# Optimization experiments

Hardware: AMD Instinct MI355X
Metric: run time of the kernel (lower is better)

Reference implementation:

```python
import jax, jax.numpy as jnp
import numpy as np
from jax import lax

B, C, H, W = 2, 256, 64, 64
CI = C // 2           # inter_channels = 128
CH = CI // 2          # key/query channels = 64
EPS = 1e-5


def conv1x1(x, w, b):
    # x: [B,C,H,W], w: [O,C], b: [O]
    return jnp.einsum('oc,bchw->bohw', w, x) + b[None, :, None, None]


def bn(x, g, be, m, v):
    inv = (g / jnp.sqrt(v + EPS))[None, :, None, None]
    return (x - m[None, :, None, None]) * inv + be[None, :, None, None]


def setup_inputs() -> dict:
    key = jax.random.key(0)
    ks = jax.random.split(key, 40)
    r = lambda i, shape, sc=0.05: jax.random.normal(ks[i], shape, dtype=jnp.float32) * sc
    u = lambda i, shape: jax.random.uniform(ks[i], shape, dtype=jnp.float32, minval=0.5, maxval=1.5)
    return {
        'q': jax.random.normal(ks[0], (B, C, H, W), dtype=jnp.float32),
        's': jax.random.normal(ks[1], (B, C, H, W), dtype=jnp.float32),
        'scale': jnp.full((1,), 0.3, dtype=jnp.float32),
        'w_v': r(2, (CI, C)), 'b_v': r(3, (CI,)),
        'w_k1': r(4, (CH, C)), 'b_k1': r(5, (CH,)),
        'w_q1': r(6, (CH, C)), 'b_q1': r(7, (CH,)),
        'w_k2': r(8, (CH, C)), 'b_k2': r(9, (CH,)),
        'w_q2': r(10, (CH, C)), 'b_q2': r(11, (CH,)),
        'w_ts': r(12, (CI, C)), 'b_ts': r(13, (CI,)),
        'g_ts': u(14, (CI,)), 'be_ts': r(15, (CI,)), 'm_ts': r(16, (CI,)), 'v_ts': u(17, (CI,)),
        'w_tq': r(18, (CI, C)), 'b_tq': r(19, (CI,)),
        'g_tq': u(20, (CI,)), 'be_tq': r(21, (CI,)), 'm_tq': r(22, (CI,)), 'v_tq': u(23, (CI,)),
        'w_cat': r(24, (CI, 2 * CI, 3, 3)),
        'g_cat': u(25, (CI,)), 'be_cat': r(26, (CI,)), 'm_cat': r(27, (CI,)), 'v_cat': u(28, (CI,)),
    }


def reference(q, s, scale, w_v, b_v, w_k1, b_k1, w_q1, b_q1, w_k2, b_k2, w_q2, b_q2,
              w_ts, b_ts, g_ts, be_ts, m_ts, v_ts,
              w_tq, b_tq, g_tq, be_tq, m_tq, v_tq,
              w_cat, g_cat, be_cat, m_cat, v_cat):
    b_, _, h, w = q.shape
    n = h * w
    # values: [B, N, CI]
    v_q = conv1x1(q, w_v, b_v).reshape(b_, CI, n).transpose(0, 2, 1)
    v_s = conv1x1(s, w_v, b_v).reshape(b_, CI, n).transpose(0, 2, 1)
    # concatenated keys/queries: [B, CI, N]
    k_x = jnp.concatenate([conv1x1(q, w_k1, b_k1), conv1x1(s, w_k2, b_k2)], axis=1).reshape(b_, CI, n)
    q_x = jnp.concatenate([conv1x1(q, w_q1, b_q1), conv1x1(s, w_q2, b_q2)], axis=1).reshape(b_, CI, n)
    # affinity: [B, N, N]
    A_s = jnp.einsum('bcn,bcm->bnm', k_x, q_x)
    attn_s = jax.nn.softmax(A_s, axis=-1)
    attn_q = jax.nn.softmax(jnp.transpose(A_s, (0, 2, 1)), axis=-1)
    # p_s: [B, N, CI] -> [B, CI, H, W]
    p_s = jnp.einsum('bnm,bmc->bnc', attn_s, v_s).transpose(0, 2, 1).reshape(b_, CI, h, w)
    s_t = bn(conv1x1(s, w_ts, b_ts), g_ts, be_ts, m_ts, v_ts)
    q_t = bn(conv1x1(q, w_tq, b_tq), g_tq, be_tq, m_tq, v_tq)
    E_s = scale[0] * p_s + s_t
    q_s_ = jnp.einsum('bnm,bmc->bnc', attn_q, v_q).transpose(0, 2, 1).reshape(b_, CI, h, w)
    E_q = scale[0] * q_s_ + q_t
    cat = jnp.concatenate([E_q, E_s], axis=1)
    conv = lax.conv_general_dilated(cat, w_cat, (1, 1), 'SAME',
                                    dimension_numbers=('NCHW', 'OIHW', 'NCHW'))
    cpam = jax.nn.relu(bn(conv, g_cat, be_cat, m_cat, v_cat))
    return (cpam, E_q, E_s)
```

## Files before the change

kernel.cpp:

```cpp
#include <hip/hip_runtime.h>
#include <hip/hip_bf16.h>

#define NPIX 4096
#define NCH  256
#define CI   128
#define EPS  1e-5f
#define SOFF 20.0f

typedef unsigned short u16;
typedef __attribute__((ext_vector_type(8))) short short8;
typedef __attribute__((ext_vector_type(4))) float f32x4;

__device__ __forceinline__ float bfu2f(u16 u) {
    union { unsigned int i; float f; } x; x.i = ((unsigned int)u) << 16; return x.f;
}
__device__ __forceinline__ u16 f2bfu(float f) {
    union { float ff; unsigned int i; } x; x.ff = f;
    unsigned int r = x.i + 0x7FFFu + ((x.i >> 16) & 1u);
    return (u16)(r >> 16);
}

__device__ __forceinline__ void gload16(const u16* g, u16* l) {
    __builtin_amdgcn_global_load_lds(
        (const __attribute__((address_space(1))) unsigned int*)g,
        (__attribute__((address_space(3))) unsigned int*)l,
        16, 0, 0);
}

__global__ __launch_bounds__(256) void prep_kernel(
    const float* __restrict__ w_v,
    const float* __restrict__ w_k1, const float* __restrict__ w_q1,
    const float* __restrict__ w_k2, const float* __restrict__ w_q2,
    const float* __restrict__ w_ts, const float* __restrict__ w_tq,
    u16* __restrict__ Wbf,
    const float* __restrict__ w_cat, u16* __restrict__ wT)
{
    const int bx = blockIdx.x;
    if (bx < 768) {
        int idx = bx * 256 + threadIdx.x;
        int src = idx / 98304;
        int r   = idx - src * 98304;
        int o   = r >> 8, c = r & 255;
        float v;
        if (o < 128)      v = w_v[(size_t)o * 256 + c];
        else if (o < 192) v = (src ? w_k2 : w_k1)[(size_t)(o - 128) * 256 + c];
        else if (o < 256) v = (src ? w_q2 : w_q1)[(size_t)(o - 192) * 256 + c];
        else              v = (src ? w_ts : w_tq)[(size_t)(o - 256) * 256 + c];
        Wbf[idx] = f2bfu(v);
    } else {
        int co = bx - 768;
        const float* srcb = w_cat + (size_t)co * 2304;
        u16* dstb = wT + (size_t)co * 2304;
        for (int t = threadIdx.x; t < 2304; t += 256) {
            int ic = t / 9, tap = t - ic * 9;
            dstb[tap * 256 + ic] = f2bfu(srcb[t]);
        }
    }
}

__global__ __launch_bounds__(256) void proj2_kernel(
    const float* __restrict__ xq, const float* __restrict__ xs,
    const u16* __restrict__ Wbf,
    const float* __restrict__ b_v,
    const float* __restrict__ b_k1, const float* __restrict__ b_q1,
    const float* __restrict__ b_k2, const float* __restrict__ b_q2,
    const float* __restrict__ b_ts, const float* __restrict__ g_ts,
    const float* __restrict__ be_ts, const float* __restrict__ m_ts,
    const float* __restrict__ v_ts,
    const float* __restrict__ b_tq, const float* __restrict__ g_tq,
    const float* __restrict__ be_tq, const float* __restrict__ m_tq,
    const float* __restrict__ v_tq,
    u16* __restrict__ kT, u16* __restrict__ qT,
    u16* __restrict__ vq, u16* __restrict__ vs,
    u16* __restrict__ tq, u16* __restrict__ ts)
{
    __shared__ u16 Xs[64 * 264];
    __shared__ u16 KQ[64 * 136];

    const int tid  = threadIdx.x;
    const int lane = tid & 63;
    const int wid  = tid >> 6;
    const int l16  = lane & 15;
    const int quad = lane >> 4;

    const int n0  = blockIdx.x * 64;
    const int bz  = blockIdx.z;
    const int b   = bz >> 1, src = bz & 1;

    const float* xg = (src ? xs : xq) + (size_t)b * NCH * NPIX + n0;
    #pragma unroll
    for (int k0 = 0; k0 < 64; k0 += 16) {
        float v[16];
        #pragma unroll
        for (int k = 0; k < 16; ++k) {
            int idx = tid + (k0 + k) * 256;
            int c = idx >> 6, n = idx & 63;
            v[k] = xg[(size_t)c * NPIX + n];
        }
        #pragma unroll
        for (int k = 0; k < 16; ++k) {
            int idx = tid + (k0 + k) * 256;
            int c = idx >> 6, n = idx & 63;
            Xs[n * 264 + c] = f2bfu(v[k]);
        }
    }
    __syncthreads();

    const u16* W = Wbf + (size_t)src * 384 * 256;
    const int o0w = wid * 96;
    const float* bk = src ? b_k2 : b_k1;
    const float* bq = src ? b_q2 : b_q1;
    const float* bt = src ? b_ts : b_tq;

    f32x4 acc[24];
    #pragma unroll
    for (int ot = 0; ot < 6; ++ot) {
        int ob = o0w + ot * 16 + quad * 4;
        const float* bp;
        if (ob < 128)      bp = b_v + ob;
        else if (ob < 192) bp = bk + (ob - 128);
        else if (ob < 256) bp = bq + (ob - 192);
        else               bp = bt + (ob - 256);
        float4 b4 = *(const float4*)bp;
        f32x4 iv = (f32x4){b4.x, b4.y, b4.z, b4.w};
        #pragma unroll
        for (int pt = 0; pt < 4; ++pt) acc[ot * 4 + pt] = iv;
    }

    #pragma unroll
    for (int kc = 0; kc < 8; ++kc) {
        short8 bfr[4];
        #pragma unroll
        for (int pt = 0; pt < 4; ++pt)
            bfr[pt] = *(const short8*)&Xs[(pt * 16 + l16) * 264 + kc * 32 + quad * 8];
        #pragma unroll
        for (int ot = 0; ot < 6; ++ot) {
            short8 a = *(const short8*)&W[(size_t)(o0w + ot * 16 + l16) * 256 + kc * 32 + quad * 8];
            #pragma unroll
            for (int pt = 0; pt < 4; ++pt)
                acc[ot * 4 + pt] = __builtin_amdgcn_mfma_f32_16x16x32_bf16(a, bfr[pt], acc[ot * 4 + pt], 0, 0, 0);
        }
    }

    #pragma unroll
    for (int ot = 0; ot < 6; ++ot) {
        int ob = o0w + ot * 16;
        #pragma unroll
        for (int pt = 0; pt < 4; ++pt) {
            int px = pt * 16 + l16;
            f32x4 v4 = acc[ot * 4 + pt];
            if (ob < 128) {
                u16* dst = src ? vs : vq;
                #pragma unroll
                for (int r = 0; r < 4; ++r)
                    dst[((size_t)b * CI + ob + quad * 4 + r) * NPIX + n0 + px] = f2bfu(v4[r]);
            } else if (ob < 256) {
                int colb = (ob < 192) ? (ob - 128) : (64 + ob - 192);
                #pragma unroll
                for (int r = 0; r < 4; ++r)
                    KQ[px * 136 + colb + quad * 4 + r] = f2bfu(v4[r]);
            } else {
                const float* g  = src ? g_ts  : g_tq;
                const float* be = src ? be_ts : be_tq;
                const float* mm = src ? m_ts  : m_tq;
                const float* vv = src ? v_ts  : v_tq;
                u16* dst = src ? ts : tq;
                #pragma unroll
                for (int r = 0; r < 4; ++r) {
                    int oc = ob - 256 + quad * 4 + r;
                    float inv = g[oc] * rsqrtf(vv[oc] + EPS);
                    dst[((size_t)b * CI + oc) * NPIX + n0 + px] =
                        f2bfu((v4[r] - mm[oc]) * inv + be[oc]);
                }
            }
        }
    }
    __syncthreads();

    const int chb = src ? 64 : 0;
    #pragma unroll
    for (int u = 0; u < 4; ++u) {
        int idx = tid + u * 256;
        int px = idx >> 4, oct = idx & 15;
        uint4 val = *(const uint4*)&KQ[px * 136 + oct * 8];
        if (oct < 8)
            *(uint4*)&kT[((size_t)b * NPIX + n0 + px) * CI + chb + oct * 8] = val;
        else
            *(uint4*)&qT[((size_t)b * NPIX + n0 + px) * CI + chb + (oct - 8) * 8] = val;
    }
}

#define AKS_OFF 0
#define AVT_OFF 16384
#define APS_OFF 32768
#define ASMEM_U16 37376

__global__ __launch_bounds__(256) void attn_kernel(
    const u16* __restrict__ kT, const u16* __restrict__ qT,
    const u16* __restrict__ vq, const u16* __restrict__ vs,
    u16* __restrict__ Opart, float* __restrict__ Lpart, int nseg)
{
    __shared__ __align__(16) u16 smem[ASMEM_U16];
    u16* Ps = smem + APS_OFF;

    const int tid  = threadIdx.x;
    const int lane = tid & 63;
    const int wid  = tid >> 6;
    const int l16  = lane & 15;
    const int quad = lane >> 4;
    const int strip = wid * 16;

    const int nt = blockIdx.x;
    const int n0 = nt * 64;
    const int at = blockIdx.y;
    const int z  = blockIdx.z;
    const int b  = z / nseg;
    const int seg = z - b * nseg;

    const u16* Qg = at ? qT : kT;
    const u16* Kg = at ? kT : qT;
    const u16* Vg = at ? vq : vs;

    short8 qf[4];
    {
        const u16* Qb = Qg + ((size_t)b * NPIX + n0 + strip + l16) * CI;
        #pragma unroll
        for (int kc = 0; kc < 4; ++kc)
            qf[kc] = *(const short8*)&Qb[kc * 32 + quad * 8];
    }

    f32x4 o[8];
    #pragma unroll
    for (int ct = 0; ct < 8; ++ct) o[ct] = (f32x4){0.f, 0.f, 0.f, 0.f};
    float L = 0.f;

    const u16* KgB = Kg + (size_t)b * NPIX * CI;
    const u16* VgB = Vg + (size_t)b * CI * NPIX;

    const int mt0 = seg * (64 / nseg);
    const int mt1 = mt0 + (64 / nseg);

    #define ISSUE_TILE(buf, m0_)                                              \
    {                                                                         \
        u16* kb_ = smem + AKS_OFF + (buf) * 8192;                             \
        u16* vb_ = smem + AVT_OFF + (buf) * 8192;                             \
        _Pragma("unroll")                                                     \
        for (int k = 0; k < 4; ++k) {                                         \
            int sb  = k * 256 + wid * 64;                                     \
            int idx = sb + lane;                                              \
            int row = idx >> 4, segp = idx & 15;                              \
            int segg = segp ^ (row & 15);                                     \
            gload16(KgB + (size_t)((m0_) + row) * CI + segg * 8, kb_ + sb * 8); \
        }                                                                     \
        _Pragma("unroll")                                                     \
        for (int k = 0; k < 4; ++k) {                                         \
            int sb  = k * 256 + wid * 64;                                     \
            int idx = sb + lane;                                              \
            int c = idx >> 3, sgp = idx & 7;                                  \
            int sgg = sgp ^ (c & 7);                                          \
            gload16(VgB + (size_t)c * NPIX + (m0_) + sgg * 8, vb_ + sb * 8);  \
        }                                                                     \
    }

    int cur = 0;
    ISSUE_TILE(0, mt0 * 64);

    for (int mt = mt0; mt < mt1; ++mt) {
        __syncthreads();
        if (mt + 1 < mt1) ISSUE_TILE(1 - cur, (mt + 1) * 64);

        const u16* Ks = smem + AKS_OFF + cur * 8192;
        const u16* Vt = smem + AVT_OFF + cur * 8192;

        f32x4 sv[4];
        #pragma unroll
        for (int m2 = 0; m2 < 4; ++m2) {
            f32x4 c = (f32x4){0.f, 0.f, 0.f, 0.f};
            #pragma unroll
            for (int kc = 0; kc < 4; ++kc) {
                int s = kc * 4 + quad;
                short8 kf = *(const short8*)&Ks[(m2 * 16 + l16) * 128 + ((s ^ l16) * 8)];
                c = __builtin_amdgcn_mfma_f32_16x16x32_bf16(kf, qf[kc], c, 0, 0, 0);
            }
            sv[m2] = c;
        }

        float Lsum = 0.f;
        u16* myPs = Ps + (strip + l16) * 72;
        #pragma unroll
        for (int m2 = 0; m2 < 4; ++m2) {
            float p0 = __expf(sv[m2][0] - SOFF);
            float p1 = __expf(sv[m2][1] - SOFF);
            float p2 = __expf(sv[m2][2] - SOFF);
            float p3 = __expf(sv[m2][3] - SOFF);
            Lsum += (p0 + p1) + (p2 + p3);
            ushort4 pk;
            pk.x = f2bfu(p0); pk.y = f2bfu(p1);
            pk.z = f2bfu(p2); pk.w = f2bfu(p3);
            *(ushort4*)&myPs[m2 * 16 + quad * 4] = pk;
        }
        Lsum += __shfl_xor(Lsum, 16);
        Lsum += __shfl_xor(Lsum, 32);
        L += Lsum;

        short8 ap[2];
        #pragma unroll
        for (int kc = 0; kc < 2; ++kc)
            ap[kc] = *(const short8*)&Ps[(strip + l16) * 72 + kc * 32 + quad * 8];
        #pragma unroll
        for (int ct = 0; ct < 8; ++ct) {
            #pragma unroll
            for (int kc = 0; kc < 2; ++kc) {
                int s = kc * 4 + quad;
                short8 bv = *(const short8*)&Vt[(ct * 16 + l16) * 64 + ((s ^ (l16 & 7)) * 8)];
                o[ct] = __builtin_amdgcn_mfma_f32_16x16x32_bf16(ap[kc], bv, o[ct], 0, 0, 0);
            }
        }
        cur ^= 1;
    }

    const size_t tile = (((size_t)(at * 2 + b) * 64 + nt) * nseg + seg);
    u16* Ob = Opart + tile * 8192;
    #pragma unroll
    for (int r = 0; r < 4; ++r) {
        int row = strip + quad * 4 + r;
        #pragma unroll
        for (int ct = 0; ct < 8; ++ct)
            Ob[row * 128 + ct * 16 + l16] = f2bfu(o[ct][r]);
    }
    if (quad == 0)
        Lpart[tile * 64 + strip + l16] = L;
    #undef ISSUE_TILE
}

__global__ __launch_bounds__(256) void attn_combine_kernel(
    const u16* __restrict__ Opart, const float* __restrict__ Lpart,
    const u16* __restrict__ tq, const u16* __restrict__ ts,
    const float* __restrict__ scale_p,
    float* __restrict__ out, u16* __restrict__ Ebf, int nseg)
{
    __shared__ float Of[128 * 68];
    __shared__ float invL[64];

    const int tid = threadIdx.x;
    const int nt = blockIdx.x;
    const int n0 = nt * 64;
    const int at = blockIdx.y;
    const int b  = blockIdx.z;

    const u16* Tg = at ? tq : ts;
    float* outE   = out + (size_t)(at ? 1 : 2) * 1048576;
    const int ch0 = at ? 0 : 128;
    const size_t tbase = ((size_t)(at * 2 + b) * 64 + nt) * nseg;

    if (tid < 64) {
        float Lg = 0.f;
        for (int s = 0; s < nseg; ++s) Lg += Lpart[(tbase + s) * 64 + tid];
        invL[tid] = 1.f / Lg;
    }
    __syncthreads();

    #pragma unroll
    for (int k = 0; k < 4; ++k) {
        int idx = tid + k * 256;
        int row = idx >> 4, oct = idx & 15;
        float m[8] = {0.f, 0.f, 0.f, 0.f, 0.f, 0.f, 0.f, 0.f};
        for (int s = 0; s < nseg; ++s) {
            union { uint4 v; u16 u[8]; } pk;
            pk.v = *(const uint4*)&Opart[(tbase + s) * 8192 + row * 128 + oct * 8];
            #pragma unroll
            for (int j = 0; j < 8; ++j) m[j] += bfu2f(pk.u[j]);
        }
        float w = invL[row];
        #pragma unroll
        for (int j = 0; j < 8; ++j)
            Of[(oct * 8 + j) * 68 + row] = m[j] * w;
    }
    __syncthreads();

    float scale = *scale_p;
    const u16* Tb = Tg + (size_t)b * CI * NPIX + n0;
    float* Ob = outE + (size_t)b * CI * NPIX + n0;
    for (int idx = tid; idx < 128 * 64; idx += 256) {
        int c = idx >> 6, r = idx & 63;
        float v = scale * Of[c * 68 + r] + bfu2f(Tb[(size_t)c * NPIX + r]);
        Ob[(size_t)c * NPIX + r] = v;
        Ebf[((size_t)b * NPIX + n0 + r) * NCH + ch0 + c] = f2bfu(v);
    }
}

#define CXT_STR 40

__global__ __launch_bounds__(256) void conv_kernel(
    const u16* __restrict__ Ebf,
    const u16* __restrict__ wT,
    const float* __restrict__ g_cat, const float* __restrict__ be_cat,
    const float* __restrict__ m_cat, const float* __restrict__ v_cat,
    float* __restrict__ out)
{
    __shared__ u16 XtW[4][3 * 34 * CXT_STR];

    const int tid  = threadIdx.x;
    const int lane = tid & 63;
    const int wid  = tid >> 6;
    const int l16  = lane & 15;
    const int quad = lane >> 4;

    const int h    = blockIdx.x;
    const int coff = blockIdx.y * 32;
    const int b    = blockIdx.z;

    const int cot = wid >> 1;
    const int pxt = (wid & 1) * 2;
    const int gc0 = pxt * 16 - 1;

    f32x4 acc[2];
    #pragma unroll
    for (int j = 0; j < 2; ++j) acc[j] = (f32x4){0.f, 0.f, 0.f, 0.f};

    const u16* Eb = Ebf + (size_t)b * NPIX * NCH;
    u16* Xw = &XtW[wid][0];
    const int cobase = coff + cot * 16 + l16;

    for (int icc = 0; icc < 8; ++icc) {
        const int ic0 = icc * 32;

        short8 wfrag[9];
        #pragma unroll
        for (int tap = 0; tap < 9; ++tap)
            wfrag[tap] = *(const short8*)&wT[((size_t)cobase * 9 + tap) * 256 + ic0 + quad * 8];

        for (int u = lane; u < 408; u += 64) {
            int part = u & 3, xe = u >> 2;
            int dh = xe / 34, x = xe - dh * 34;
            int gr = h + dh - 1, gc = gc0 + x;
            uint4 val = make_uint4(0u, 0u, 0u, 0u);
            if ((unsigned)gr < 64u && (unsigned)gc < 64u)
                val = *(const uint4*)&Eb[((size_t)gr * 64 + gc) * NCH + ic0 + part * 8];
            *(uint4*)&Xw[(dh * 34 + x) * CXT_STR + part * 8] = val;
        }

        #pragma unroll
        for (int tap = 0; tap < 9; ++tap) {
            const int dh = tap / 3, dw = tap % 3;
            short8 bf[2];
            #pragma unroll
            for (int j = 0; j < 2; ++j) {
                int x = j * 16 + l16 + dw;
                bf[j] = *(const short8*)&Xw[(dh * 34 + x) * CXT_STR + quad * 8];
            }
            #pragma unroll
            for (int j = 0; j < 2; ++j)
                acc[j] = __builtin_amdgcn_mfma_f32_16x16x32_bf16(wfrag[tap], bf[j], acc[j], 0, 0, 0);
        }
    }

    #pragma unroll
    for (int r = 0; r < 4; ++r) {
        int co = coff + cot * 16 + quad * 4 + r;
        float inv = g_cat[co] * rsqrtf(v_cat[co] + EPS);
        float mm  = m_cat[co];
        float be  = be_cat[co];
        #pragma unroll
        for (int j = 0; j < 2; ++j) {
            int wcol = (pxt + j) * 16 + l16;
            float v = (acc[j][r] - mm) * inv + be;
            out[((size_t)b * CI + co) * NPIX + h * 64 + wcol] = fmaxf(v, 0.f);
        }
    }
}

extern "C" void kernel_launch(void* const* d_in, const int* in_sizes, int n_in,
                              void* d_out, int out_size, void* d_ws, size_t ws_size,
                              hipStream_t stream)
{
    const float* q     = (const float*)d_in[0];
    const float* s     = (const float*)d_in[1];
    const float* scale = (const float*)d_in[2];
    const float* w_v   = (const float*)d_in[3];
    const float* b_v   = (const float*)d_in[4];
    const float* w_k1  = (const float*)d_in[5];
    const float* b_k1  = (const float*)d_in[6];
    const float* w_q1  = (const float*)d_in[7];
    const float* b_q1  = (const float*)d_in[8];
    const float* w_k2  = (const float*)d_in[9];
    const float* b_k2  = (const float*)d_in[10];
    const float* w_q2  = (const float*)d_in[11];
    const float* b_q2  = (const float*)d_in[12];
    const float* w_ts  = (const float*)d_in[13];
    const float* b_ts  = (const float*)d_in[14];
    const float* g_ts  = (const float*)d_in[15];
    const float* be_ts = (const float*)d_in[16];
    const float* m_ts  = (const float*)d_in[17];
    const float* v_ts  = (const float*)d_in[18];
    const float* w_tq  = (const float*)d_in[19];
    const float* b_tq  = (const float*)d_in[20];
    const float* g_tq  = (const float*)d_in[21];
    const float* be_tq = (const float*)d_in[22];
    const float* m_tq  = (const float*)d_in[23];
    const float* v_tq  = (const float*)d_in[24];
    const float* w_cat = (const float*)d_in[25];
    const float* g_cat = (const float*)d_in[26];
    const float* be_cat= (const float*)d_in[27];
    const float* m_cat = (const float*)d_in[28];
    const float* v_cat = (const float*)d_in[29];

    float* out = (float*)d_out;
    u16* ws = (u16*)d_ws;
    const size_t SZ = (size_t)2 * CI * NPIX;
    u16* kT  = ws;
    u16* qT  = kT + SZ;
    u16* vq  = qT + SZ;
    u16* vs  = vq + SZ;
    u16* tq  = vs + SZ;
    u16* ts  = tq + SZ;
    u16* Wbf = ts + SZ;
    u16* B   = Wbf + 196608;
    u16* Ebf = B;
    u16* wTc = B + 2097152;
    u16* Opart = wTc + 294912;

    const size_t fixed_u16 = 6 * SZ + 196608 + 2097152 + 294912;
    int nseg = 1;
    {
        size_t need4 = (fixed_u16 + (size_t)4 * 2097152) * 2 + (size_t)4 * 131072;
        size_t need2 = (fixed_u16 + (size_t)2 * 2097152) * 2 + (size_t)2 * 131072;
        if (ws_size >= need4)      nseg = 4;
        else if (ws_size >= need2) nseg = 2;
    }
    float* Lpart = (float*)(Opart + (size_t)nseg * 256 * 8192);

    dim3 blk(256);
    hipLaunchKernelGGL(prep_kernel, dim3(896), blk, 0, stream,
                       w_v, w_k1, w_q1, w_k2, w_q2, w_ts, w_tq, Wbf, w_cat, wTc);
    hipLaunchKernelGGL(proj2_kernel, dim3(64, 1, 4), blk, 0, stream,
                       q, s, Wbf, b_v, b_k1, b_q1, b_k2, b_q2,
                       b_ts, g_ts, be_ts, m_ts, v_ts,
                       b_tq, g_tq, be_tq, m_tq, v_tq,
                       kT, qT, vq, vs, tq, ts);
    hipLaunchKernelGGL(attn_kernel, dim3(64, 2, 2 * nseg), blk, 0, stream,
                       kT, qT, vq, vs, Opart, Lpart, nseg);
    hipLaunchKernelGGL(attn_combine_kernel, dim3(64, 2, 2), blk, 0, stream,
                       Opart, Lpart, tq, ts, scale, out, Ebf, nseg);
    hipLaunchKernelGGL(conv_kernel, dim3(64, 4, 2), blk, 0, stream,
                       Ebf, wTc, g_cat, be_cat, m_cat, v_cat, out);
}
```

Before: 243.0 us.

## Switch attention to 32x32x16 MFMA with 2x2 wave tiling and coalesce E store

The attention kernel moves from 16x16x32 to 32x32x16 bf16 MFMA. Each wave now computes a 32-row by 32-key score block and a 32-row by 64-channel output block, rather than a 16-row strip over all keys and channels. The goal is fewer MFMA issues and fewer LDS fragment loads per FLOP. The cost is an extra __syncthreads per tile so waves can share the P matrix, plus an LDS reduction of the row sums across wave pairs. The combine kernel also stages E in shared memory so the bf16 pixel-major output is written with coalesced channel-contiguous stores.

```diff
diff --git a/kernel.cpp b/kernel.cpp
--- a/kernel.cpp
+++ b/kernel.cpp
@@ -10,6 +10,7 @@
 typedef unsigned short u16;
 typedef __attribute__((ext_vector_type(8))) short short8;
 typedef __attribute__((ext_vector_type(4))) float f32x4;
+typedef __attribute__((ext_vector_type(16))) float f32x16;
 
 __device__ __forceinline__ float bfu2f(u16 u) {
     union { unsigned int i; float f; } x; x.i = ((unsigned int)u) << 16; return x.f;
@@ -195,20 +196,24 @@
 #define APS_OFF 32768
 #define ASMEM_U16 37376
 
-__global__ __launch_bounds__(256) void attn_kernel(
+__global__ __launch_bounds__(256, 2) void attn_kernel(
     const u16* __restrict__ kT, const u16* __restrict__ qT,
     const u16* __restrict__ vq, const u16* __restrict__ vs,
     u16* __restrict__ Opart, float* __restrict__ Lpart, int nseg)
 {
     __shared__ __align__(16) u16 smem[ASMEM_U16];
+    __shared__ float Lbuf[2][2][32];
     u16* Ps = smem + APS_OFF;
 
     const int tid  = threadIdx.x;
     const int lane = tid & 63;
     const int wid  = tid >> 6;
-    const int l16  = lane & 15;
-    const int quad = lane >> 4;
-    const int strip = wid * 16;
+    const int l32  = lane & 31;
+    const int hi   = lane >> 5;
+    const int rg   = wid >> 1;
+    const int mh   = wid & 1;
+    const int chb  = (wid & 1) * 64;
+    const int rows0 = rg * 32;
 
     const int nt = blockIdx.x;
     const int n0 = nt * 64;
@@ -221,18 +226,20 @@
     const u16* Kg = at ? kT : qT;
     const u16* Vg = at ? vq : vs;
 
-    short8 qf[4];
+    short8 qf[8];
     {
-        const u16* Qb = Qg + ((size_t)b * NPIX + n0 + strip + l16) * CI;
-        #pragma unroll
-        for (int kc = 0; kc < 4; ++kc)
-            qf[kc] = *(const short8*)&Qb[kc * 32 + quad * 8];
-    }
-
-    f32x4 o[8];
-    #pragma unroll
-    for (int ct = 0; ct < 8; ++ct) o[ct] = (f32x4){0.f, 0.f, 0.f, 0.f};
-    float L = 0.f;
+        const u16* Qb = Qg + ((size_t)b * NPIX + n0 + rows0 + l32) * CI;
+        #pragma unroll
+        for (int kc = 0; kc < 8; ++kc)
+            qf[kc] = *(const short8*)&Qb[kc * 16 + hi * 8];
+    }
+
+    f32x16 o2[2];
+    #pragma unroll
+    for (int ct = 0; ct < 2; ++ct)
+        #pragma unroll
+        for (int i = 0; i < 16; ++i) o2[ct][i] = 0.f;
+    float Lacc = 0.f;
 
     const u16* KgB = Kg + (size_t)b * NPIX * CI;
     const u16* VgB = Vg + (size_t)b * CI * NPIX;
@@ -272,48 +279,49 @@
         const u16* Ks = smem + AKS_OFF + cur * 8192;
         const u16* Vt = smem + AVT_OFF + cur * 8192;
 
-        f32x4 sv[4];
-        #pragma unroll
-        for (int m2 = 0; m2 < 4; ++m2) {
-            f32x4 c = (f32x4){0.f, 0.f, 0.f, 0.f};
-            #pragma unroll
-            for (int kc = 0; kc < 4; ++kc) {
-                int s = kc * 4 + quad;
-                short8 kf = *(const short8*)&Ks[(m2 * 16 + l16) * 128 + ((s ^ l16) * 8)];
-                c = __builtin_amdgcn_mfma_f32_16x16x32_bf16(kf, qf[kc], c, 0, 0, 0);
+        f32x16 sv;
+        #pragma unroll
+        for (int i = 0; i < 16; ++i) sv[i] = 0.f;
+        {
+            const int row = mh * 32 + l32;
+            #pragma unroll
+            for (int kc = 0; kc < 8; ++kc) {
+                int sg = (kc * 2 + hi) ^ (row & 15);
+                short8 kf = *(const short8*)&Ks[row * 128 + sg * 8];
+                sv = __builtin_amdgcn_mfma_f32_32x32x16_bf16(kf, qf[kc], sv, 0, 0, 0);
             }
-            sv[m2] = c;
-        }
-
-        float Lsum = 0.f;
-        u16* myPs = Ps + (strip + l16) * 72;
-        #pragma unroll
-        for (int m2 = 0; m2 < 4; ++m2) {
-            float p0 = __expf(sv[m2][0] - SOFF);
-            float p1 = __expf(sv[m2][1] - SOFF);
-            float p2 = __expf(sv[m2][2] - SOFF);
-            float p3 = __expf(sv[m2][3] - SOFF);
-            Lsum += (p0 + p1) + (p2 + p3);
+        }
+
+        float Ls = 0.f;
+        u16* myPs = Ps + (rows0 + l32) * 72 + mh * 32;
+        #pragma unroll
+        for (int rq = 0; rq < 4; ++rq) {
+            float p0 = __expf(sv[rq * 4 + 0] - SOFF);
+            float p1 = __expf(sv[rq * 4 + 1] - SOFF);
+            float p2 = __expf(sv[rq * 4 + 2] - SOFF);
+            float p3 = __expf(sv[rq * 4 + 3] - SOFF);
+            Ls += (p0 + p1) + (p2 + p3);
             ushort4 pk;
             pk.x = f2bfu(p0); pk.y = f2bfu(p1);
             pk.z = f2bfu(p2); pk.w = f2bfu(p3);
-            *(ushort4*)&myPs[m2 * 16 + quad * 4] = pk;
-        }
-        Lsum += __shfl_xor(Lsum, 16);
-        Lsum += __shfl_xor(Lsum, 32);
-        L += Lsum;
-
-        short8 ap[2];
-        #pragma unroll
-        for (int kc = 0; kc < 2; ++kc)
-            ap[kc] = *(const short8*)&Ps[(strip + l16) * 72 + kc * 32 + quad * 8];
-        #pragma unroll
-        for (int ct = 0; ct < 8; ++ct) {
-            #pragma unroll
-            for (int kc = 0; kc < 2; ++kc) {
-                int s = kc * 4 + quad;
-                short8 bv = *(const short8*)&Vt[(ct * 16 + l16) * 64 + ((s ^ (l16 & 7)) * 8)];
-                o[ct] = __builtin_amdgcn_mfma_f32_16x16x32_bf16(ap[kc], bv, o[ct], 0, 0, 0);
+            *(ushort4*)&myPs[rq * 8 + hi * 4] = pk;
+        }
+        Ls += __shfl_xor(Ls, 32);
+        Lacc += Ls;
+        __syncthreads();
+
+        short8 pf[4];
+        #pragma unroll
+        for (int kc = 0; kc < 4; ++kc)
+            pf[kc] = *(const short8*)&Ps[(rows0 + l32) * 72 + kc * 16 + hi * 8];
+        #pragma unroll
+        for (int ct = 0; ct < 2; ++ct) {
+            const int c = chb + ct * 32 + l32;
+            #pragma unroll
+            for (int kc = 0; kc < 4; ++kc) {
+                int slot = (kc * 2 + hi) ^ (c & 7);
+                short8 vf = *(const short8*)&Vt[c * 64 + slot * 8];
+                o2[ct] = __builtin_amdgcn_mfma_f32_32x32x16_bf16(vf, pf[kc], o2[ct], 0, 0, 0);
             }
         }
         cur ^= 1;
@@ -321,15 +329,25 @@
 
     const size_t tile = (((size_t)(at * 2 + b) * 64 + nt) * nseg + seg);
     u16* Ob = Opart + tile * 8192;
-    #pragma unroll
-    for (int r = 0; r < 4; ++r) {
-        int row = strip + quad * 4 + r;
-        #pragma unroll
-        for (int ct = 0; ct < 8; ++ct)
-            Ob[row * 128 + ct * 16 + l16] = f2bfu(o[ct][r]);
-    }
-    if (quad == 0)
-        Lpart[tile * 64 + strip + l16] = L;
+    {
+        const int row = rows0 + l32;
+        #pragma unroll
+        for (int ct = 0; ct < 2; ++ct) {
+            #pragma unroll
+            for (int rq = 0; rq < 4; ++rq) {
+                ushort4 pk;
+                pk.x = f2bfu(o2[ct][rq * 4 + 0]);
+                pk.y = f2bfu(o2[ct][rq * 4 + 1]);
+                pk.z = f2bfu(o2[ct][rq * 4 + 2]);
+                pk.w = f2bfu(o2[ct][rq * 4 + 3]);
+                *(ushort4*)&Ob[row * 128 + chb + ct * 32 + rq * 8 + hi * 4] = pk;
+            }
+        }
+    }
+    if (hi == 0) Lbuf[rg][mh][l32] = Lacc;
+    __syncthreads();
+    if (mh == 0 && hi == 0)
+        Lpart[tile * 64 + rows0 + l32] = Lbuf[rg][0][l32] + Lbuf[rg][1][l32];
     #undef ISSUE_TILE
 }
 
@@ -385,7 +403,13 @@
         int c = idx >> 6, r = idx & 63;
         float v = scale * Of[c * 68 + r] + bfu2f(Tb[(size_t)c * NPIX + r]);
         Ob[(size_t)c * NPIX + r] = v;
-        Ebf[((size_t)b * NPIX + n0 + r) * NCH + ch0 + c] = f2bfu(v);
+        Of[c * 68 + r] = v;
+    }
+    __syncthreads();
+    u16* Eb = Ebf + ((size_t)b * NPIX + n0) * NCH + ch0;
+    for (int idx = tid; idx < 128 * 64; idx += 256) {
+        int r = idx >> 7, c = idx & 127;
+        Eb[(size_t)r * NCH + c] = f2bfu(Of[c * 68 + r]);
     }
 }
 
```

Measured after the change: 248.5 us. 2.3% more time.

## Split projection, combine and conv kernels into more, smaller blocks

Applied to the files above, without the earlier changes.

Splits the projection kernel's output channels across two blocks, one producing keys and the other queries, and halves the row tile in the combine kernel. The combine kernel also now stages its results in shared memory so the bf16 channel-last writes to Ebf are coalesced. The conv kernel gives each block 16 output channels and each wave one 16-pixel strip. The aim is more blocks per kernel to fill the GPU's compute units, plus better-coalesced stores. In exchange, each input tile is reloaded by more blocks and per-wave reuse of conv weights and inputs drops.

```diff
diff --git a/kernel.cpp b/kernel.cpp
--- a/kernel.cpp
+++ b/kernel.cpp
@@ -75,7 +75,7 @@
     u16* __restrict__ tq, u16* __restrict__ ts)
 {
     __shared__ u16 Xs[64 * 264];
-    __shared__ u16 KQ[64 * 136];
+    __shared__ u16 KQ[64 * 72];
 
     const int tid  = threadIdx.x;
     const int lane = tid & 63;
@@ -84,6 +84,7 @@
     const int quad = lane >> 4;
 
     const int n0  = blockIdx.x * 64;
+    const int oh  = blockIdx.y;
     const int bz  = blockIdx.z;
     const int b   = bz >> 1, src = bz & 1;
 
@@ -107,14 +108,14 @@
     __syncthreads();
 
     const u16* W = Wbf + (size_t)src * 384 * 256;
-    const int o0w = wid * 96;
+    const int o0w = oh * 192 + wid * 48;
     const float* bk = src ? b_k2 : b_k1;
     const float* bq = src ? b_q2 : b_q1;
     const float* bt = src ? b_ts : b_tq;
 
-    f32x4 acc[24];
-    #pragma unroll
-    for (int ot = 0; ot < 6; ++ot) {
+    f32x4 acc[12];
+    #pragma unroll
+    for (int ot = 0; ot < 3; ++ot) {
         int ob = o0w + ot * 16 + quad * 4;
         const float* bp;
         if (ob < 128)      bp = b_v + ob;
@@ -134,7 +135,7 @@
         for (int pt = 0; pt < 4; ++pt)
             bfr[pt] = *(const short8*)&Xs[(pt * 16 + l16) * 264 + kc * 32 + quad * 8];
         #pragma unroll
-        for (int ot = 0; ot < 6; ++ot) {
+        for (int ot = 0; ot < 3; ++ot) {
             short8 a = *(const short8*)&W[(size_t)(o0w + ot * 16 + l16) * 256 + kc * 32 + quad * 8];
             #pragma unroll
             for (int pt = 0; pt < 4; ++pt)
@@ -143,7 +144,7 @@
     }
 
     #pragma unroll
-    for (int ot = 0; ot < 6; ++ot) {
+    for (int ot = 0; ot < 3; ++ot) {
         int ob = o0w + ot * 16;
         #pragma unroll
         for (int pt = 0; pt < 4; ++pt) {
@@ -155,10 +156,10 @@
                 for (int r = 0; r < 4; ++r)
                     dst[((size_t)b * CI + ob + quad * 4 + r) * NPIX + n0 + px] = f2bfu(v4[r]);
             } else if (ob < 256) {
-                int colb = (ob < 192) ? (ob - 128) : (64 + ob - 192);
+                int colb = (ob < 192) ? (ob - 128) : (ob - 192);
                 #pragma unroll
                 for (int r = 0; r < 4; ++r)
-                    KQ[px * 136 + colb + quad * 4 + r] = f2bfu(v4[r]);
+                    KQ[px * 72 + colb + quad * 4 + r] = f2bfu(v4[r]);
             } else {
                 const float* g  = src ? g_ts  : g_tq;
                 const float* be = src ? be_ts : be_tq;
@@ -177,16 +178,14 @@
     }
     __syncthreads();
 
+    u16* KQdst = oh ? qT : kT;
     const int chb = src ? 64 : 0;
     #pragma unroll
-    for (int u = 0; u < 4; ++u) {
+    for (int u = 0; u < 2; ++u) {
         int idx = tid + u * 256;
-        int px = idx >> 4, oct = idx & 15;
-        uint4 val = *(const uint4*)&KQ[px * 136 + oct * 8];
-        if (oct < 8)
-            *(uint4*)&kT[((size_t)b * NPIX + n0 + px) * CI + chb + oct * 8] = val;
-        else
-            *(uint4*)&qT[((size_t)b * NPIX + n0 + px) * CI + chb + (oct - 8) * 8] = val;
+        int px = idx >> 3, oct = idx & 7;
+        uint4 val = *(const uint4*)&KQ[px * 72 + oct * 8];
+        *(uint4*)&KQdst[((size_t)b * NPIX + n0 + px) * CI + chb + oct * 8] = val;
     }
 }
 
@@ -339,53 +338,62 @@
     const float* __restrict__ scale_p,
     float* __restrict__ out, u16* __restrict__ Ebf, int nseg)
 {
-    __shared__ float Of[128 * 68];
-    __shared__ float invL[64];
+    __shared__ float Of[128 * 36];
+    __shared__ float invL[32];
 
     const int tid = threadIdx.x;
-    const int nt = blockIdx.x;
-    const int n0 = nt * 64;
-    const int at = blockIdx.y;
-    const int b  = blockIdx.z;
+    const int bx  = blockIdx.x;
+    const int nt  = bx >> 1;
+    const int rh  = bx & 1;
+    const int n0  = nt * 64;
+    const int r0  = rh * 32;
+    const int at  = blockIdx.y;
+    const int b   = blockIdx.z;
 
     const u16* Tg = at ? tq : ts;
     float* outE   = out + (size_t)(at ? 1 : 2) * 1048576;
     const int ch0 = at ? 0 : 128;
     const size_t tbase = ((size_t)(at * 2 + b) * 64 + nt) * nseg;
 
-    if (tid < 64) {
+    if (tid < 32) {
         float Lg = 0.f;
-        for (int s = 0; s < nseg; ++s) Lg += Lpart[(tbase + s) * 64 + tid];
+        for (int s = 0; s < nseg; ++s) Lg += Lpart[(tbase + s) * 64 + r0 + tid];
         invL[tid] = 1.f / Lg;
     }
     __syncthreads();
 
     #pragma unroll
-    for (int k = 0; k < 4; ++k) {
+    for (int k = 0; k < 2; ++k) {
         int idx = tid + k * 256;
-        int row = idx >> 4, oct = idx & 15;
+        int rl = idx >> 4, oct = idx & 15;
         float m[8] = {0.f, 0.f, 0.f, 0.f, 0.f, 0.f, 0.f, 0.f};
         for (int s = 0; s < nseg; ++s) {
             union { uint4 v; u16 u[8]; } pk;
-            pk.v = *(const uint4*)&Opart[(tbase + s) * 8192 + row * 128 + oct * 8];
+            pk.v = *(const uint4*)&Opart[(tbase + s) * 8192 + (r0 + rl) * 128 + oct * 8];
             #pragma unroll
             for (int j = 0; j < 8; ++j) m[j] += bfu2f(pk.u[j]);
         }
-        float w = invL[row];
+        float w = invL[rl];
         #pragma unroll
         for (int j = 0; j < 8; ++j)
-            Of[(oct * 8 + j) * 68 + row] = m[j] * w;
+            Of[(oct * 8 + j) * 36 + rl] = m[j] * w;
     }
     __syncthreads();
 
     float scale = *scale_p;
-    const u16* Tb = Tg + (size_t)b * CI * NPIX + n0;
-    float* Ob = outE + (size_t)b * CI * NPIX + n0;
-    for (int idx = tid; idx < 128 * 64; idx += 256) {
-        int c = idx >> 6, r = idx & 63;
-        float v = scale * Of[c * 68 + r] + bfu2f(Tb[(size_t)c * NPIX + r]);
-        Ob[(size_t)c * NPIX + r] = v;
-        Ebf[((size_t)b * NPIX + n0 + r) * NCH + ch0 + c] = f2bfu(v);
+    const u16* Tb = Tg + (size_t)b * CI * NPIX + n0 + r0;
+    float* Ob = outE + (size_t)b * CI * NPIX + n0 + r0;
+    for (int idx = tid; idx < 128 * 32; idx += 256) {
+        int c = idx >> 5, rl = idx & 31;
+        float v = scale * Of[c * 36 + rl] + bfu2f(Tb[(size_t)c * NPIX + rl]);
+        Ob[(size_t)c * NPIX + rl] = v;
+        Of[c * 36 + rl] = v;
+    }
+    __syncthreads();
+    u16* Eb = Ebf + ((size_t)b * NPIX + n0 + r0) * NCH + ch0;
+    for (int idx = tid; idx < 128 * 32; idx += 256) {
+        int rl = idx >> 7, c = idx & 127;
+        Eb[(size_t)rl * NCH + c] = f2bfu(Of[c * 36 + rl]);
     }
 }
 
@@ -398,7 +406,7 @@
     const float* __restrict__ m_cat, const float* __restrict__ v_cat,
     float* __restrict__ out)
 {
-    __shared__ u16 XtW[4][3 * 34 * CXT_STR];
+    __shared__ u16 XtW[4][3 * 18 * CXT_STR];
 
     const int tid  = threadIdx.x;
     const int lane = tid & 63;
@@ -407,20 +415,16 @@
     const int quad = lane >> 4;
 
     const int h    = blockIdx.x;
-    const int coff = blockIdx.y * 32;
+    const int co0  = blockIdx.y * 16;
     const int b    = blockIdx.z;
 
-    const int cot = wid >> 1;
-    const int pxt = (wid & 1) * 2;
-    const int gc0 = pxt * 16 - 1;
-
-    f32x4 acc[2];
-    #pragma unroll
-    for (int j = 0; j < 2; ++j) acc[j] = (f32x4){0.f, 0.f, 0.f, 0.f};
+    const int gc0 = wid * 16 - 1;
+
+    f32x4 acc = (f32x4){0.f, 0.f, 0.f, 0.f};
 
     const u16* Eb = Ebf + (size_t)b * NPIX * NCH;
     u16* Xw = &XtW[wid][0];
-    const int cobase = coff + cot * 16 + l16;
+    const int cobase = co0 + l16;
 
     for (int icc = 0; icc < 8; ++icc) {
         const int ic0 = icc * 32;
@@ -430,43 +434,33 @@
         for (int tap = 0; tap < 9; ++tap)
             wfrag[tap] = *(const short8*)&wT[((size_t)cobase * 9 + tap) * 256 + ic0 + quad * 8];
 
-        for (int u = lane; u < 408; u += 64) {
+        for (int u = lane; u < 216; u += 64) {
             int part = u & 3, xe = u >> 2;
-            int dh = xe / 34, x = xe - dh * 34;
+            int dh = xe / 18, x = xe - dh * 18;
             int gr = h + dh - 1, gc = gc0 + x;
             uint4 val = make_uint4(0u, 0u, 0u, 0u);
             if ((unsigned)gr < 64u && (unsigned)gc < 64u)
                 val = *(const uint4*)&Eb[((size_t)gr * 64 + gc) * NCH + ic0 + part * 8];
-            *(uint4*)&Xw[(dh * 34 + x) * CXT_STR + part * 8] = val;
+            *(uint4*)&Xw[(dh * 18 + x) * CXT_STR + part * 8] = val;
         }
 
         #pragma unroll
         for (int tap = 0; tap < 9; ++tap) {
             const int dh = tap / 3, dw = tap % 3;
-            short8 bf[2];
-            #pragma unroll
-            for (int j = 0; j < 2; ++j) {
-                int x = j * 16 + l16 + dw;
-                bf[j] = *(const short8*)&Xw[(dh * 34 + x) * CXT_STR + quad * 8];
-            }
-            #pragma unroll
-            for (int j = 0; j < 2; ++j)
-                acc[j] = __builtin_amdgcn_mfma_f32_16x16x32_bf16(wfrag[tap], bf[j], acc[j], 0, 0, 0);
+            short8 bf = *(const short8*)&Xw[(dh * 18 + l16 + dw) * CXT_STR + quad * 8];
+            acc = __builtin_amdgcn_mfma_f32_16x16x32_bf16(wfrag[tap], bf, acc, 0, 0, 0);
         }
     }
 
     #pragma unroll
     for (int r = 0; r < 4; ++r) {
-        int co = coff + cot * 16 + quad * 4 + r;
+        int co = co0 + quad * 4 + r;
         float inv = g_cat[co] * rsqrtf(v_cat[co] + EPS);
         float mm  = m_cat[co];
         float be  = be_cat[co];
-        #pragma unroll
-        for (int j = 0; j < 2; ++j) {
-            int wcol = (pxt + j) * 16 + l16;
-            float v = (acc[j][r] - mm) * inv + be;
-            out[((size_t)b * CI + co) * NPIX + h * 64 + wcol] = fmaxf(v, 0.f);
-        }
+        int wcol = wid * 16 + l16;
+        float v = (acc[r] - mm) * inv + be;
+        out[((size_t)b * CI + co) * NPIX + h * 64 + wcol] = fmaxf(v, 0.f);
     }
 }
 
@@ -533,15 +527,15 @@
     dim3 blk(256);
     hipLaunchKernelGGL(prep_kernel, dim3(896), blk, 0, stream,
                        w_v, w_k1, w_q1, w_k2, w_q2, w_ts, w_tq, Wbf, w_cat, wTc);
-    hipLaunchKernelGGL(proj2_kernel, dim3(64, 1, 4), blk, 0, stream,
+    hipLaunchKernelGGL(proj2_kernel, dim3(64, 2, 4), blk, 0, stream,
                        q, s, Wbf, b_v, b_k1, b_q1, b_k2, b_q2,
                        b_ts, g_ts, be_ts, m_ts, v_ts,
                        b_tq, g_tq, be_tq, m_tq, v_tq,
                        kT, qT, vq, vs, tq, ts);
     hipLaunchKernelGGL(attn_kernel, dim3(64, 2, 2 * nseg), blk, 0, stream,
                        kT, qT, vq, vs, Opart, Lpart, nseg);
-    hipLaunchKernelGGL(attn_combine_kernel, dim3(64, 2, 2), blk, 0, stream,
+    hipLaunchKernelGGL(attn_combine_kernel, dim3(128, 2, 2), blk, 0, stream,
                        Opart, Lpart, tq, ts, scale, out, Ebf, nseg);
-    hipLaunchKernelGGL(conv_kernel, dim3(64, 4, 2), blk, 0, stream,
+    hipLaunchKernelGGL(conv_kernel, dim3(64, 8, 2), blk, 0, stream,
                        Ebf, wTc, g_cat, be_cat, m_cat, v_cat, out);
 }
```

Result: no change. 243.2 us (+0.1%).
